# Kernel tuning notes

Measured on AMD Instinct MI355X. Metric: run time of the kernel, lower is better.

The kernel has to match this reference:

```python
import jax, jax.numpy as jnp
import numpy as np

NUM_HEADS = 8
LN_EPS = 1e-5


def _layer_norm(x, g, b):
    mu = jnp.mean(x, axis=-1, keepdims=True)
    var = jnp.mean(jnp.square(x - mu), axis=-1, keepdims=True)
    return (x - mu) * jax.lax.rsqrt(var + LN_EPS) * g + b


def setup_inputs() -> dict:
    key = jax.random.key(0)
    ks = jax.random.split(key, 8)
    B, N, D = 8, 2048, 256
    s = 0.02
    return {
        "x": jax.random.normal(ks[0], (B, N, D), jnp.float32),
        "pos": jax.random.normal(ks[1], (B, N, 2 * D), jnp.float32),
        "mask": jax.random.randint(ks[2], (B, N), 0, 2) > 0,  # True = padded key
        "Wqkv": jax.random.normal(ks[3], (D, 3 * D), jnp.float32) * s,
        "bqkv": jnp.zeros((3 * D,), jnp.float32),
        "Wpos": jax.random.normal(ks[4], (2 * D, 2 * D), jnp.float32) * s,
        "bpos": jnp.zeros((2 * D,), jnp.float32),
        "ln1_g": jnp.ones((D,), jnp.float32),
        "ln1_b": jnp.zeros((D,), jnp.float32),
        "W1": jax.random.normal(ks[5], (D, 4 * D), jnp.float32) * s,
        "b1": jnp.zeros((4 * D,), jnp.float32),
        "W2": jax.random.normal(ks[6], (4 * D, D), jnp.float32) * s,
        "b2": jnp.zeros((D,), jnp.float32),
        "ln2_g": jnp.ones((D,), jnp.float32),
        "ln2_b": jnp.zeros((D,), jnp.float32),
    }


def reference(x, pos, mask, Wqkv, bqkv, Wpos, bpos, ln1_g, ln1_b,
              W1, b1, W2, b2, ln2_g, ln2_b):
    B, N, D = x.shape
    H = NUM_HEADS
    Dh = D // H

    qkv = x @ Wqkv + bqkv                      # [B,N,3D]
    q, k, v = jnp.split(qkv, 3, axis=-1)       # each [B,N,D]
    qk_pos = pos @ Wpos + bpos                 # [B,N,2D]
    q_pos, k_pos = jnp.split(qk_pos, 2, axis=-1)
    q = q + q_pos
    k = k + k_pos

    # [B,N,D] -> [B,H,N,Dh]
    q = q.reshape(B, N, H, Dh).transpose(0, 2, 1, 3)
    k = k.reshape(B, N, H, Dh).transpose(0, 2, 1, 3)
    v = v.reshape(B, N, H, Dh).transpose(0, 2, 1, 3)

    scores = jnp.einsum('bhqd,bhkd->bhqk', q, k) / jnp.sqrt(jnp.float32(Dh))
    scores = jnp.where(mask[:, None, None, :], -jnp.inf, scores)
    attn = jax.nn.softmax(scores, axis=-1)
    out = jnp.einsum('bhqk,bhkd->bhqd', attn, v)
    out = out.transpose(0, 2, 1, 3).reshape(B, N, D)

    h = _layer_norm(x + out, ln1_g, ln1_b)
    ffn = jax.nn.relu(h @ W1 + b1) @ W2 + b2
    return _layer_norm(h + ffn, ln2_g, ln2_b)
```

## Files before the change

kernel.cpp:

```cpp
#include <hip/hip_runtime.h>
#include <math.h>

#define BATCH 8
#define SEQ   2048
#define DIM   256
#define NHEAD 8
#define DHEAD 32
#define MROWS (BATCH*SEQ)
#define KCAT  768

typedef short bf16x8 __attribute__((ext_vector_type(8)));
typedef float f32x4  __attribute__((ext_vector_type(4)));
typedef float f32x16 __attribute__((ext_vector_type(16)));

#define CLSCALE 0.25503485f

static __device__ __forceinline__ float exp2_raw(float x) {
    float r;
    asm("v_exp_f32 %0, %1" : "=v"(r) : "v"(x));
    return r;
}

static __device__ __forceinline__ unsigned bf16rne(float f) {
    unsigned u = __float_as_uint(f);
    return (u + 0x7FFFu + ((u >> 16) & 1u)) >> 16;
}

__global__ __launch_bounds__(256) void convcat_kernel(
    const float* __restrict__ x, const float* __restrict__ pos,
    unsigned short* __restrict__ acat, int n1, int n2)
{
    int i = blockIdx.x * 256 + threadIdx.x;
    const float* s; size_t dst; int j;
    if (i < n1) {
        j = i; s = x;
        int row = j >> 5, c8 = (j & 31) * 8;
        dst = (size_t)row * KCAT + c8;
    } else {
        j = i - n1; if (j >= n2) return; s = pos;
        int row = j >> 6, c8 = (j & 63) * 8;
        dst = (size_t)row * KCAT + 256 + c8;
    }
    float4 a = ((const float4*)s)[2 * j];
    float4 b = ((const float4*)s)[2 * j + 1];
    union { unsigned short u[8]; uint4 v; } o;
    o.u[0] = bf16rne(a.x); o.u[1] = bf16rne(a.y);
    o.u[2] = bf16rne(a.z); o.u[3] = bf16rne(a.w);
    o.u[4] = bf16rne(b.x); o.u[5] = bf16rne(b.y);
    o.u[6] = bf16rne(b.z); o.u[7] = bf16rne(b.w);
    *(uint4*)&acat[dst] = o.v;
}

__global__ __launch_bounds__(256) void wtrans_all_kernel(
    const float* __restrict__ Wqkv, const float* __restrict__ Wpos,
    const float* __restrict__ W1, const float* __restrict__ W2,
    unsigned short* __restrict__ wqk, unsigned short* __restrict__ wv,
    unsigned short* __restrict__ w1, unsigned short* __restrict__ w2)
{
    int b = blockIdx.x;
    const float* src; unsigned short* dst;
    int srcN, srcColOff, dstK, dstKOff, nbx;
    if (b < 128)      {          src = Wqkv; dst = wqk; srcN = 768;  srcColOff = 0;   dstK = 768;  dstKOff = 0;   nbx = 16; }
    else if (b < 384) { b -= 128; src = Wpos; dst = wqk; srcN = 512;  srcColOff = 0;   dstK = 768;  dstKOff = 256; nbx = 16; }
    else if (b < 448) { b -= 384; src = Wqkv; dst = wv;  srcN = 768;  srcColOff = 512; dstK = 256;  dstKOff = 0;   nbx = 8;  }
    else if (b < 704) { b -= 448; src = W1;   dst = w1;  srcN = 1024; srcColOff = 0;   dstK = 256;  dstKOff = 0;   nbx = 32; }
    else              { b -= 704; src = W2;   dst = w2;  srcN = 256;  srcColOff = 0;   dstK = 1024; dstKOff = 0;   nbx = 8;  }
    const int tn0 = (b % nbx) * 32;
    const int tk0 = (b / nbx) * 32;

    __shared__ float tile[32][33];
    const int tx = threadIdx.x & 31;
    const int ty = threadIdx.x >> 5;
    #pragma unroll
    for (int r = ty; r < 32; r += 8)
        tile[r][tx] = src[(size_t)(tk0 + r) * srcN + srcColOff + tn0 + tx];
    __syncthreads();
    #pragma unroll
    for (int r = ty; r < 32; r += 8)
        dst[(size_t)(tn0 + r) * dstK + dstKOff + tk0 + tx] =
            (unsigned short)bf16rne(tile[tx][r]);
}

template<int MODE>
static __device__ __forceinline__ void mgemm_body(
    int bx, int by,
    const unsigned short* __restrict__ A, const unsigned short* __restrict__ Wt,
    const float* __restrict__ bias, const float* __restrict__ bias2,
    float* __restrict__ C, unsigned short* __restrict__ Cb,
    int M, int K, int Nc, int lda,
    unsigned short* __restrict__ u0, unsigned short* __restrict__ u1,
    unsigned short* __restrict__ u2)
{
    const int t    = threadIdx.x;
    const int wv   = t >> 6;
    const int lane = t & 63;
    const int g    = lane >> 4;
    const int lo   = lane & 15;
    const int wr   = wv >> 1;
    const int wc   = wv & 1;
    const int r0   = by * 128 + wr * 64;
    const int c0   = bx * 128 + wc * 64;

    f32x4 acc[4][4];
    #pragma unroll
    for (int i = 0; i < 4; ++i)
        #pragma unroll
        for (int j = 0; j < 4; ++j)
            #pragma unroll
            for (int r = 0; r < 4; ++r) acc[i][j][r] = 0.f;

    const unsigned short* aP[4];
    const unsigned short* bP[4];
    #pragma unroll
    for (int i = 0; i < 4; ++i) {
        aP[i] = A  + (size_t)(r0 + 16 * i + lo) * lda + g * 8;
        bP[i] = Wt + (size_t)(c0 + 16 * i + lo) * K + g * 8;
    }

    bf16x8 aA[4], bA[4], aB[4], bB[4];
    #pragma unroll
    for (int i = 0; i < 4; ++i) {
        aA[i] = *(const bf16x8*)(aP[i]);
        bA[i] = *(const bf16x8*)(bP[i]);
    }

    for (int k0 = 0; k0 < K; k0 += 64) {
        #pragma unroll
        for (int i = 0; i < 4; ++i) {
            aB[i] = *(const bf16x8*)(aP[i] + k0 + 32);
            bB[i] = *(const bf16x8*)(bP[i] + k0 + 32);
        }
        #pragma unroll
        for (int i = 0; i < 4; ++i)
            #pragma unroll
            for (int j = 0; j < 4; ++j)
                acc[i][j] = __builtin_amdgcn_mfma_f32_16x16x32_bf16(
                    aA[i], bA[j], acc[i][j], 0, 0, 0);
        if (k0 + 64 < K) {
            #pragma unroll
            for (int i = 0; i < 4; ++i) {
                aA[i] = *(const bf16x8*)(aP[i] + k0 + 64);
                bA[i] = *(const bf16x8*)(bP[i] + k0 + 64);
            }
        }
        #pragma unroll
        for (int i = 0; i < 4; ++i)
            #pragma unroll
            for (int j = 0; j < 4; ++j)
                acc[i][j] = __builtin_amdgcn_mfma_f32_16x16x32_bf16(
                    aB[i], bB[j], acc[i][j], 0, 0, 0);
    }

    #pragma unroll
    for (int j = 0; j < 4; ++j) {
        const int col = c0 + 16 * j + lo;
        const float bs = bias[col] + ((MODE == 4) ? bias2[col] : 0.f);
        #pragma unroll
        for (int i = 0; i < 4; ++i) {
            if (MODE == 5) {
                const int row0 = r0 + 16 * i + g * 4;
                const int bb   = row0 >> 11;
                const int nn0  = row0 & (SEQ - 1);
                const int hh   = col >> 5;
                const int dh   = col & 31;
                uint2 pk;
                pk.x = bf16rne(acc[i][j][0] + bs) | (bf16rne(acc[i][j][1] + bs) << 16);
                pk.y = bf16rne(acc[i][j][2] + bs) | (bf16rne(acc[i][j][3] + bs) << 16);
                *(uint2*)&u2[(((size_t)bb * NHEAD + hh) * DHEAD + dh) * SEQ + nn0] = pk;
            } else {
                #pragma unroll
                for (int r = 0; r < 4; ++r) {
                    const int row = r0 + 16 * i + g * 4 + r;
                    float v = acc[i][j][r] + bs;
                    if (MODE == 0) {
                        C[(size_t)row * Nc + col] = v;
                    } else if (MODE == 1) {
                        Cb[(size_t)row * Nc + col] =
                            (unsigned short)bf16rne(fmaxf(v, 0.f));
                    } else {
                        const int bb = row >> 11;
                        const int nn = row & (SEQ - 1);
                        const int which = col >> 8;
                        const int d  = col & 255;
                        const int hh = d >> 5;
                        const int dh = d & 31;
                        const size_t dst =
                            (((size_t)bb * NHEAD + hh) * SEQ + nn) * DHEAD + dh;
                        if (which == 0) {
                            u0[dst] = (unsigned short)bf16rne(v * CLSCALE);
                        } else {
                            u1[dst] = (unsigned short)bf16rne(v);
                        }
                    }
                }
            }
        }
    }
}

template<int MODE>
__global__ __launch_bounds__(256, 3) void mgemm_kernel(
    const unsigned short* __restrict__ A, const unsigned short* __restrict__ Wt,
    const float* __restrict__ bias, const float* __restrict__ bias2,
    float* __restrict__ C, unsigned short* __restrict__ Cb,
    int M, int K, int Nc, int lda,
    unsigned short* __restrict__ u0, unsigned short* __restrict__ u1,
    unsigned short* __restrict__ u2)
{
    mgemm_body<MODE>(blockIdx.x, blockIdx.y, A, Wt, bias, bias2, C, Cb,
                     M, K, Nc, lda, u0, u1, u2);
}

__global__ __launch_bounds__(256, 3) void qkv_kernel(
    const unsigned short* __restrict__ acat,
    const unsigned short* __restrict__ wqk, const unsigned short* __restrict__ wv,
    const float* __restrict__ bqkv, const float* __restrict__ bpos,
    unsigned short* __restrict__ qb, unsigned short* __restrict__ kb,
    unsigned short* __restrict__ vt)
{
    const int b = blockIdx.x;
    if (b < 512) {
        mgemm_body<4>(b & 3, b >> 2, acat, wqk, bqkv, bpos, nullptr, nullptr,
                      MROWS, KCAT, 512, KCAT, qb, kb, nullptr);
    } else {
        const int b2 = b - 512;
        mgemm_body<5>(b2 & 1, b2 >> 1, acat, wv, bqkv + 512, nullptr,
                      nullptr, nullptr, MROWS, 256, 256, KCAT,
                      nullptr, nullptr, vt);
    }
}

__global__ __launch_bounds__(256) void attn_kernel(
    const unsigned short* __restrict__ Qb, const unsigned short* __restrict__ Kb,
    const unsigned short* __restrict__ Vt, const int* __restrict__ mask,
    float* __restrict__ O)
{
    __shared__ float bias_s[SEQ];

    const int t    = threadIdx.x;
    const int wv   = t >> 6;
    const int lane = t & 63;
    const int h    = lane >> 5;
    const int ql   = lane & 31;

    const int sb   = ((blockIdx.x & 7) << 6) | (blockIdx.x >> 3);
    const int bh   = sb >> 3;
    const int qblk = sb & 7;
    const int bb   = bh >> 3;
    const int hh   = bh & 7;
    const int qt   = qblk * 256 + wv * 64;

    const int* mrow = mask + bb * SEQ;
    for (int i = t; i < SEQ; i += 256)
        bias_s[i] = mrow[i] ? -3.0e38f : 0.0f;
    __syncthreads();

    const unsigned short* Qh = Qb + (size_t)bh * SEQ * 32;
    const unsigned short* Kh = Kb + (size_t)bh * SEQ * 32;
    const unsigned short* Vh = Vt + (size_t)bh * 32 * SEQ;

    bf16x8 qf[2][2];
    #pragma unroll
    for (int i = 0; i < 2; ++i)
        #pragma unroll
        for (int dh = 0; dh < 2; ++dh)
            qf[i][dh] = *(const bf16x8*)&Qh[(size_t)(qt + 32 * i + ql) * 32 + 16 * dh + 8 * h];

    f32x16 acc[2];
    #pragma unroll
    for (int i = 0; i < 2; ++i)
        #pragma unroll
        for (int r = 0; r < 16; ++r) acc[i][r] = 0.f;
    float l[2] = {0.f, 0.f};

    bf16x8 kf0 = *(const bf16x8*)&Kh[(size_t)ql * 32 + 8 * h];
    bf16x8 kf1 = *(const bf16x8*)&Kh[(size_t)ql * 32 + 16 + 8 * h];
    bf16x8 vf0 = *(const bf16x8*)&Vh[(size_t)ql * SEQ + 8 * h];
    bf16x8 vf1 = *(const bf16x8*)&Vh[(size_t)ql * SEQ + 16 + 8 * h];

    for (int k0 = 0; k0 < SEQ; k0 += 32) {
        const int kn = (k0 + 32) & (SEQ - 1);
        bf16x8 nkf0 = *(const bf16x8*)&Kh[(size_t)(kn + ql) * 32 + 8 * h];
        bf16x8 nkf1 = *(const bf16x8*)&Kh[(size_t)(kn + ql) * 32 + 16 + 8 * h];
        bf16x8 nvf0 = *(const bf16x8*)&Vh[(size_t)ql * SEQ + kn + 8 * h];
        bf16x8 nvf1 = *(const bf16x8*)&Vh[(size_t)ql * SEQ + kn + 16 + 8 * h];

        f32x16 cbv;
        #pragma unroll
        for (int c = 0; c < 4; ++c) {
            f32x4 cb = *(const f32x4*)&bias_s[k0 + 4 * h + 8 * c];
            #pragma unroll
            for (int e = 0; e < 4; ++e) cbv[4 * c + e] = cb[e];
        }

        #pragma unroll
        for (int i = 0; i < 2; ++i) {
            __builtin_amdgcn_s_setprio(1);
            f32x16 s = __builtin_amdgcn_mfma_f32_32x32x16_bf16(
                kf0, qf[i][0], cbv, 0, 0, 0);
            s = __builtin_amdgcn_mfma_f32_32x32x16_bf16(
                kf1, qf[i][1], s, 0, 0, 0);
            __builtin_amdgcn_s_setprio(0);

            float p[16];
            float tl = 0.f;
            #pragma unroll
            for (int r = 0; r < 16; ++r) {
                p[r] = exp2_raw(s[r]);
                tl += p[r];
            }
            l[i] += tl;

            unsigned w00, w01, w10, w11, w20, w21, w30, w31;
            asm("v_cvt_pk_bf16_f32 %0, %1, %2" : "=v"(w00) : "v"(p[0]),  "v"(p[1]));
            asm("v_cvt_pk_bf16_f32 %0, %1, %2" : "=v"(w01) : "v"(p[2]),  "v"(p[3]));
            asm("v_cvt_pk_bf16_f32 %0, %1, %2" : "=v"(w10) : "v"(p[4]),  "v"(p[5]));
            asm("v_cvt_pk_bf16_f32 %0, %1, %2" : "=v"(w11) : "v"(p[6]),  "v"(p[7]));
            asm("v_cvt_pk_bf16_f32 %0, %1, %2" : "=v"(w20) : "v"(p[8]),  "v"(p[9]));
            asm("v_cvt_pk_bf16_f32 %0, %1, %2" : "=v"(w21) : "v"(p[10]), "v"(p[11]));
            asm("v_cvt_pk_bf16_f32 %0, %1, %2" : "=v"(w30) : "v"(p[12]), "v"(p[13]));
            asm("v_cvt_pk_bf16_f32 %0, %1, %2" : "=v"(w31) : "v"(p[14]), "v"(p[15]));
            asm volatile("v_permlane32_swap_b32 %0, %1" : "+v"(w00), "+v"(w10));
            asm volatile("v_permlane32_swap_b32 %0, %1" : "+v"(w01), "+v"(w11));
            asm volatile("v_permlane32_swap_b32 %0, %1" : "+v"(w20), "+v"(w30));
            asm volatile("v_permlane32_swap_b32 %0, %1" : "+v"(w21), "+v"(w31));
            union { unsigned u[4]; bf16x8 v; } pa, pb;
            pa.u[0] = w00; pa.u[1] = w01; pa.u[2] = w10; pa.u[3] = w11;
            pb.u[0] = w20; pb.u[1] = w21; pb.u[2] = w30; pb.u[3] = w31;

            __builtin_amdgcn_s_setprio(1);
            acc[i] = __builtin_amdgcn_mfma_f32_32x32x16_bf16(
                vf0, pa.v, acc[i], 0, 0, 0);
            acc[i] = __builtin_amdgcn_mfma_f32_32x32x16_bf16(
                vf1, pb.v, acc[i], 0, 0, 0);
            __builtin_amdgcn_s_setprio(0);
        }

        kf0 = nkf0; kf1 = nkf1; vf0 = nvf0; vf1 = nvf1;
    }

    #pragma unroll
    for (int i = 0; i < 2; ++i) {
        l[i] += __shfl_xor(l[i], 32);
        const float inv = (l[i] > 0.f) ? 1.0f / l[i] : 0.f;
        const size_t rowoff = (size_t)(bb * SEQ + qt + 32 * i + ql) * DIM + hh * 32;
        #pragma unroll
        for (int c = 0; c < 4; ++c) {
            float4 ov;
            ov.x = acc[i][4 * c + 0] * inv;
            ov.y = acc[i][4 * c + 1] * inv;
            ov.z = acc[i][4 * c + 2] * inv;
            ov.w = acc[i][4 * c + 3] * inv;
            *(float4*)&O[rowoff + 4 * h + 8 * c] = ov;
        }
    }
}

__global__ __launch_bounds__(256) void ln_kernel(
    const float* __restrict__ X, const float* __restrict__ R,
    const float* __restrict__ gam, const float* __restrict__ bet,
    float* __restrict__ Y, unsigned short* __restrict__ Yb)
{
    const int lane = threadIdx.x & 63;
    const int row  = blockIdx.x * 4 + (threadIdx.x >> 6);
    const size_t off = (size_t)row * DIM + lane * 4;

    float4 xv = *(const float4*)&X[off];
    float4 rv = *(const float4*)&R[off];
    float4 v;
    v.x = xv.x + rv.x; v.y = xv.y + rv.y;
    v.z = xv.z + rv.z; v.w = xv.w + rv.w;

    float s = (v.x + v.y) + (v.z + v.w);
    #pragma unroll
    for (int o = 1; o < 64; o <<= 1) s += __shfl_xor(s, o);
    const float mu = s * (1.f / 256.f);

    float4 d;
    d.x = v.x - mu; d.y = v.y - mu; d.z = v.z - mu; d.w = v.w - mu;
    float s2 = (d.x * d.x + d.y * d.y) + (d.z * d.z + d.w * d.w);
    #pragma unroll
    for (int o = 1; o < 64; o <<= 1) s2 += __shfl_xor(s2, o);
    const float rs = rsqrtf(s2 * (1.f / 256.f) + 1e-5f);

    float4 gv = *(const float4*)&gam[lane * 4];
    float4 bv = *(const float4*)&bet[lane * 4];
    float4 y;
    y.x = d.x * rs * gv.x + bv.x;
    y.y = d.y * rs * gv.y + bv.y;
    y.z = d.z * rs * gv.z + bv.z;
    y.w = d.w * rs * gv.w + bv.w;
    *(float4*)&Y[off] = y;

    if (Yb) {
        uint2 pk;
        pk.x = bf16rne(y.x) | (bf16rne(y.y) << 16);
        pk.y = bf16rne(y.z) | (bf16rne(y.w) << 16);
        *(uint2*)&Yb[off] = pk;
    }
}

extern "C" void kernel_launch(void* const* d_in, const int* in_sizes, int n_in,
                              void* d_out, int out_size, void* d_ws, size_t ws_size,
                              hipStream_t stream)
{
    const float* x    = (const float*)d_in[0];
    const float* pos  = (const float*)d_in[1];
    const int*   mask = (const int*)d_in[2];
    const float* Wqkv = (const float*)d_in[3];
    const float* bqkv = (const float*)d_in[4];
    const float* Wpos = (const float*)d_in[5];
    const float* bpos = (const float*)d_in[6];
    const float* ln1g = (const float*)d_in[7];
    const float* ln1b = (const float*)d_in[8];
    const float* W1   = (const float*)d_in[9];
    const float* b1   = (const float*)d_in[10];
    const float* W2   = (const float*)d_in[11];
    const float* b2   = (const float*)d_in[12];
    const float* ln2g = (const float*)d_in[13];
    const float* ln2b = (const float*)d_in[14];
    float* out = (float*)d_out;

    char* base = (char*)d_ws;
    const size_t MB = 1024 * 1024;
    const size_t SZ = (size_t)MROWS * DIM;
    unsigned short* acat = (unsigned short*)(base + 0);
    float*          ao   = (float*)(base + 0);
    unsigned short* mid  = (unsigned short*)(base + 0);
    unsigned short* qb   = (unsigned short*)(base + 34 * MB);
    unsigned short* kb   = (unsigned short*)(base + 42 * MB);
    unsigned short* vt   = (unsigned short*)(base + 58 * MB);
    unsigned short* hb   = (unsigned short*)(base + 66 * MB);
    float*          hbuf = (float*)(base + 74 * MB);
    unsigned short* wqk  = (unsigned short*)(base + 90 * MB);
    unsigned short* wv   = wqk + 512 * 768;
    unsigned short* w1   = wv + 256 * 256;
    unsigned short* w2   = w1 + 1024 * 256;
    float*          f2   = out;

    dim3 blk(256);

    convcat_kernel<<<dim3((3 * (int)(SZ / 8)) / 256), blk, 0, stream>>>(
        x, pos, acat, (int)(SZ / 8), (int)(2 * SZ / 8));
    wtrans_all_kernel<<<dim3(960), blk, 0, stream>>>(
        Wqkv, Wpos, W1, W2, wqk, wv, w1, w2);
    qkv_kernel<<<dim3(768), blk, 0, stream>>>(
        acat, wqk, wv, bqkv, bpos, qb, kb, vt);
    attn_kernel<<<dim3(BATCH * NHEAD * (SEQ / 256)), blk, 0, stream>>>(
        qb, kb, vt, mask, ao);
    ln_kernel<<<dim3(MROWS / 4), blk, 0, stream>>>(x, ao, ln1g, ln1b, hbuf, hb);
    mgemm_kernel<1><<<dim3(1024 / 128, MROWS / 128), blk, 0, stream>>>(
        hb, w1, b1, nullptr, nullptr, mid, MROWS, 256, 1024, 256,
        nullptr, nullptr, nullptr);
    mgemm_kernel<0><<<dim3(256 / 128, MROWS / 128), blk, 0, stream>>>(
        mid, w2, b2, nullptr, f2, nullptr, MROWS, 1024, 256, 1024,
        nullptr, nullptr, nullptr);
    ln_kernel<<<dim3(MROWS / 4), blk, 0, stream>>>(hbuf, f2, ln2g, ln2b, out, nullptr);
}
```

Before: 235.5 us.

## Split attention keys into two halves and combine partials in LN1

```diff
diff --git a/kernel.cpp b/kernel.cpp
--- a/kernel.cpp
+++ b/kernel.cpp
@@ -8,6 +8,7 @@
 #define DHEAD 32
 #define MROWS (BATCH*SEQ)
 #define KCAT  768
+#define SZE   ((size_t)MROWS * DIM)
 
 typedef short bf16x8 __attribute__((ext_vector_type(8)));
 typedef float f32x4  __attribute__((ext_vector_type(4)));
@@ -233,7 +234,7 @@
 __global__ __launch_bounds__(256) void attn_kernel(
     const unsigned short* __restrict__ Qb, const unsigned short* __restrict__ Kb,
     const unsigned short* __restrict__ Vt, const int* __restrict__ mask,
-    float* __restrict__ O)
+    float* __restrict__ accP, float* __restrict__ lP)
 {
     __shared__ float bias_s[SEQ];
 
@@ -243,12 +244,14 @@
     const int h    = lane >> 5;
     const int ql   = lane & 31;
 
-    const int sb   = ((blockIdx.x & 7) << 6) | (blockIdx.x >> 3);
-    const int bh   = sb >> 3;
-    const int qblk = sb & 7;
+    const int sb   = ((blockIdx.x & 7) << 7) | (blockIdx.x >> 3);
+    const int bh   = sb >> 4;
+    const int qblk = (sb >> 1) & 7;
+    const int kh   = sb & 1;
     const int bb   = bh >> 3;
     const int hh   = bh & 7;
     const int qt   = qblk * 256 + wv * 64;
+    const int khoff = kh * (SEQ / 2);
 
     const int* mrow = mask + bb * SEQ;
     for (int i = t; i < SEQ; i += 256)
@@ -273,12 +276,12 @@
         for (int r = 0; r < 16; ++r) acc[i][r] = 0.f;
     float l[2] = {0.f, 0.f};
 
-    bf16x8 kf0 = *(const bf16x8*)&Kh[(size_t)ql * 32 + 8 * h];
-    bf16x8 kf1 = *(const bf16x8*)&Kh[(size_t)ql * 32 + 16 + 8 * h];
-    bf16x8 vf0 = *(const bf16x8*)&Vh[(size_t)ql * SEQ + 8 * h];
-    bf16x8 vf1 = *(const bf16x8*)&Vh[(size_t)ql * SEQ + 16 + 8 * h];
-
-    for (int k0 = 0; k0 < SEQ; k0 += 32) {
+    bf16x8 kf0 = *(const bf16x8*)&Kh[(size_t)(khoff + ql) * 32 + 8 * h];
+    bf16x8 kf1 = *(const bf16x8*)&Kh[(size_t)(khoff + ql) * 32 + 16 + 8 * h];
+    bf16x8 vf0 = *(const bf16x8*)&Vh[(size_t)ql * SEQ + khoff + 8 * h];
+    bf16x8 vf1 = *(const bf16x8*)&Vh[(size_t)ql * SEQ + khoff + 16 + 8 * h];
+
+    for (int k0 = khoff; k0 < khoff + SEQ / 2; k0 += 32) {
         const int kn = (k0 + 32) & (SEQ - 1);
         bf16x8 nkf0 = *(const bf16x8*)&Kh[(size_t)(kn + ql) * 32 + 8 * h];
         bf16x8 nkf1 = *(const bf16x8*)&Kh[(size_t)(kn + ql) * 32 + 16 + 8 * h];
@@ -339,25 +342,28 @@
         kf0 = nkf0; kf1 = nkf1; vf0 = nvf0; vf1 = nvf1;
     }
 
+    float* accH = accP + (size_t)kh * SZE;
     #pragma unroll
     for (int i = 0; i < 2; ++i) {
         l[i] += __shfl_xor(l[i], 32);
-        const float inv = (l[i] > 0.f) ? 1.0f / l[i] : 0.f;
+        if (h == 0)
+            lP[(size_t)kh * 64 * SEQ + (size_t)bh * SEQ + qt + 32 * i + ql] = l[i];
         const size_t rowoff = (size_t)(bb * SEQ + qt + 32 * i + ql) * DIM + hh * 32;
         #pragma unroll
         for (int c = 0; c < 4; ++c) {
             float4 ov;
-            ov.x = acc[i][4 * c + 0] * inv;
-            ov.y = acc[i][4 * c + 1] * inv;
-            ov.z = acc[i][4 * c + 2] * inv;
-            ov.w = acc[i][4 * c + 3] * inv;
-            *(float4*)&O[rowoff + 4 * h + 8 * c] = ov;
+            ov.x = acc[i][4 * c + 0];
+            ov.y = acc[i][4 * c + 1];
+            ov.z = acc[i][4 * c + 2];
+            ov.w = acc[i][4 * c + 3];
+            *(float4*)&accH[rowoff + 4 * h + 8 * c] = ov;
         }
     }
 }
 
-__global__ __launch_bounds__(256) void ln_kernel(
-    const float* __restrict__ X, const float* __restrict__ R,
+__global__ __launch_bounds__(256) void ln1c_kernel(
+    const float* __restrict__ X, const float* __restrict__ accP,
+    const float* __restrict__ lP,
     const float* __restrict__ gam, const float* __restrict__ bet,
     float* __restrict__ Y, unsigned short* __restrict__ Yb)
 {
@@ -365,11 +371,21 @@
     const int row  = blockIdx.x * 4 + (threadIdx.x >> 6);
     const size_t off = (size_t)row * DIM + lane * 4;
 
+    const int hd  = lane >> 3;
+    const int bbv = row >> 11;
+    const int nn  = row & (SEQ - 1);
+    const size_t bhn = ((size_t)bbv * NHEAD + hd) * SEQ + nn;
+    const float ls = lP[bhn] + lP[(size_t)64 * SEQ + bhn];
+    const float inv = (ls > 0.f) ? 1.0f / ls : 0.f;
+
     float4 xv = *(const float4*)&X[off];
-    float4 rv = *(const float4*)&R[off];
+    float4 a0 = *(const float4*)&accP[off];
+    float4 a1 = *(const float4*)&accP[SZE + off];
     float4 v;
-    v.x = xv.x + rv.x; v.y = xv.y + rv.y;
-    v.z = xv.z + rv.z; v.w = xv.w + rv.w;
+    v.x = xv.x + (a0.x + a1.x) * inv;
+    v.y = xv.y + (a0.y + a1.y) * inv;
+    v.z = xv.z + (a0.z + a1.z) * inv;
+    v.w = xv.w + (a0.w + a1.w) * inv;
 
     float s = (v.x + v.y) + (v.z + v.w);
     #pragma unroll
@@ -392,12 +408,47 @@
     y.w = d.w * rs * gv.w + bv.w;
     *(float4*)&Y[off] = y;
 
-    if (Yb) {
-        uint2 pk;
-        pk.x = bf16rne(y.x) | (bf16rne(y.y) << 16);
-        pk.y = bf16rne(y.z) | (bf16rne(y.w) << 16);
-        *(uint2*)&Yb[off] = pk;
-    }
+    uint2 pk;
+    pk.x = bf16rne(y.x) | (bf16rne(y.y) << 16);
+    pk.y = bf16rne(y.z) | (bf16rne(y.w) << 16);
+    *(uint2*)&Yb[off] = pk;
+}
+
+__global__ __launch_bounds__(256) void ln_kernel(
+    const float* __restrict__ X, const float* __restrict__ R,
+    const float* __restrict__ gam, const float* __restrict__ bet,
+    float* __restrict__ Y)
+{
+    const int lane = threadIdx.x & 63;
+    const int row  = blockIdx.x * 4 + (threadIdx.x >> 6);
+    const size_t off = (size_t)row * DIM + lane * 4;
+
+    float4 xv = *(const float4*)&X[off];
+    float4 rv = *(const float4*)&R[off];
+    float4 v;
+    v.x = xv.x + rv.x; v.y = xv.y + rv.y;
+    v.z = xv.z + rv.z; v.w = xv.w + rv.w;
+
+    float s = (v.x + v.y) + (v.z + v.w);
+    #pragma unroll
+    for (int o = 1; o < 64; o <<= 1) s += __shfl_xor(s, o);
+    const float mu = s * (1.f / 256.f);
+
+    float4 d;
+    d.x = v.x - mu; d.y = v.y - mu; d.z = v.z - mu; d.w = v.w - mu;
+    float s2 = (d.x * d.x + d.y * d.y) + (d.z * d.z + d.w * d.w);
+    #pragma unroll
+    for (int o = 1; o < 64; o <<= 1) s2 += __shfl_xor(s2, o);
+    const float rs = rsqrtf(s2 * (1.f / 256.f) + 1e-5f);
+
+    float4 gv = *(const float4*)&gam[lane * 4];
+    float4 bv = *(const float4*)&bet[lane * 4];
+    float4 y;
+    y.x = d.x * rs * gv.x + bv.x;
+    y.y = d.y * rs * gv.y + bv.y;
+    y.z = d.z * rs * gv.z + bv.z;
+    y.w = d.w * rs * gv.w + bv.w;
+    *(float4*)&Y[off] = y;
 }
 
 extern "C" void kernel_launch(void* const* d_in, const int* in_sizes, int n_in,
@@ -423,9 +474,8 @@
 
     char* base = (char*)d_ws;
     const size_t MB = 1024 * 1024;
-    const size_t SZ = (size_t)MROWS * DIM;
     unsigned short* acat = (unsigned short*)(base + 0);
-    float*          ao   = (float*)(base + 0);
+    float*          accP = (float*)(base + 0);
     unsigned short* mid  = (unsigned short*)(base + 0);
     unsigned short* qb   = (unsigned short*)(base + 34 * MB);
     unsigned short* kb   = (unsigned short*)(base + 42 * MB);
@@ -436,24 +486,26 @@
     unsigned short* wv   = wqk + 512 * 768;
     unsigned short* w1   = wv + 256 * 256;
     unsigned short* w2   = w1 + 1024 * 256;
+    float*          lP   = (float*)(base + 93 * MB);
     float*          f2   = out;
 
     dim3 blk(256);
 
-    convcat_kernel<<<dim3((3 * (int)(SZ / 8)) / 256), blk, 0, stream>>>(
-        x, pos, acat, (int)(SZ / 8), (int)(2 * SZ / 8));
+    convcat_kernel<<<dim3((3 * (int)(SZE / 8)) / 256), blk, 0, stream>>>(
+        x, pos, acat, (int)(SZE / 8), (int)(2 * SZE / 8));
     wtrans_all_kernel<<<dim3(960), blk, 0, stream>>>(
         Wqkv, Wpos, W1, W2, wqk, wv, w1, w2);
     qkv_kernel<<<dim3(768), blk, 0, stream>>>(
         acat, wqk, wv, bqkv, bpos, qb, kb, vt);
-    attn_kernel<<<dim3(BATCH * NHEAD * (SEQ / 256)), blk, 0, stream>>>(
-        qb, kb, vt, mask, ao);
-    ln_kernel<<<dim3(MROWS / 4), blk, 0, stream>>>(x, ao, ln1g, ln1b, hbuf, hb);
+    attn_kernel<<<dim3(1024), blk, 0, stream>>>(
+        qb, kb, vt, mask, accP, lP);
+    ln1c_kernel<<<dim3(MROWS / 4), blk, 0, stream>>>(
+        x, accP, lP, ln1g, ln1b, hbuf, hb);
     mgemm_kernel<1><<<dim3(1024 / 128, MROWS / 128), blk, 0, stream>>>(
         hb, w1, b1, nullptr, nullptr, mid, MROWS, 256, 1024, 256,
         nullptr, nullptr, nullptr);
     mgemm_kernel<0><<<dim3(256 / 128, MROWS / 128), blk, 0, stream>>>(
         mid, w2, b2, nullptr, f2, nullptr, MROWS, 1024, 256, 1024,
         nullptr, nullptr, nullptr);
-    ln_kernel<<<dim3(MROWS / 4), blk, 0, stream>>>(hbuf, f2, ln2g, ln2b, out, nullptr);
-}
+    ln_kernel<<<dim3(MROWS / 4), blk, 0, stream>>>(hbuf, f2, ln2g, ln2b, out);
+}
```

Result: no change. 236.0 us (+0.2%).
